# Kernel tuning notes

Hardware: AMD Instinct MI355X
Metric: run time of the kernel (lower is better)

## Reference

```python
import jax, jax.numpy as jnp
import numpy as np
from jax import lax

N_CLS = 4
ALPHA = 1.0
EPS = 1e-4


def _level_loss(logit, prob_gt, coord_gt, weight_cls):
    # logit: [B, N_cls*A, D, H, W]; prob_gt: [B, A, D, H, W]; coord_gt: [B, K, 4] int
    B, C, D, H, W = logit.shape
    A = C // N_CLS
    logit6 = logit.reshape(B, N_CLS, A, D, H, W)
    prob = jnp.clip(jax.nn.sigmoid(logit6), EPS, 1.0 - EPS)  # [B,N_cls,A,D,H,W]
    prob_max = jnp.max(prob, axis=1)                          # [B,A,D,H,W]

    # --- negative (background) focal term with NMS peak masking ---
    negmask = (prob_gt == -1.0).astype(logit.dtype)
    pooled = lax.reduce_window(prob_max, -jnp.inf, lax.max,
                               (1, 1, 3, 3, 3), (1, 1, 1, 1, 1),
                               [(0, 0), (0, 0), (1, 1), (1, 1), (1, 1)])
    max_filter = lax.stop_gradient((pooled == prob_max).astype(logit.dtype))
    thresh_filter = (prob_max > EPS).astype(logit.dtype)
    negmask = negmask * max_filter * thresh_filter
    w_neg = lax.stop_gradient(prob_max) ** ALPHA * negmask
    loss_neg = -jnp.sum(jnp.log(1.0 - prob_max) * w_neg)
    count_neg = jnp.sum(w_neg)

    # --- positive + other-class terms at sparse GT coordinates (vmapped over batch) ---
    def per_item(p_pred, l_pred, c_gt, p_gt):
        # p_pred/l_pred: [N_cls,A,D,H,W]; c_gt: [K,4]; p_gt: [A,D,H,W]
        valid = c_gt[:, 0] > -1
        vmask = valid.astype(p_pred.dtype)
        c = jnp.where(valid[:, None], c_gt, 0)  # safe indices for padded rows
        a, d, h, w = c[:, 0], c[:, 1], c[:, 2], c[:, 3]
        cls_gt = jnp.clip(p_gt[a, d, h, w].astype(jnp.int32) - 1, 0, N_CLS - 1)  # [K]
        p_t = p_pred[cls_gt, a, d, h, w]  # [K]
        l_t = l_pred[cls_gt, a, d, h, w]
        w_pos = (1.0 - lax.stop_gradient(p_t)) ** ALPHA * weight_cls[cls_gt] * vmask
        loss_pos = -jnp.sum(jax.nn.log_sigmoid(l_t) * w_pos)
        count_pos = jnp.sum(w_pos)
        # other-class suppression
        p_o = p_pred[:, a, d, h, w]  # [N_cls, K]
        l_o = l_pred[:, a, d, h, w]
        w_o = lax.stop_gradient(
            jax.nn.relu(p_o - (p_t - 0.05))
            * (p_o > 0.5).astype(p_o.dtype)
            * (p_t > 0.5).astype(p_o.dtype))
        # torch: weight[cls_gt] = 0  -> zero entire rows for classes present among valid GTs
        present = jnp.zeros((N_CLS,), p_pred.dtype).at[cls_gt].max(vmask)
        w_o = w_o * (1.0 - present)[:, None] * vmask[None, :]
        loss_other = jnp.sum(-jax.nn.log_sigmoid(-l_o) * w_o)
        count_other = jnp.sum(w_o)
        return loss_pos, count_pos, loss_other, count_other

    lp, cp, lo, co = jax.vmap(per_item)(prob, logit6, coord_gt, prob_gt)
    return (jnp.sum(lp), loss_neg, jnp.sum(lo), jnp.sum(cp), count_neg, jnp.sum(co))


def _forward(logits0, logits1, gtprob0, gtprob1, coords0, coords1, weight_cls):
    r0 = _level_loss(logits0, gtprob0, coords0, weight_cls)
    r1 = _level_loss(logits1, gtprob1, coords1, weight_cls)
    # [loss_pos, loss_neg, loss_other, count_pos, count_neg, count_other]
    return jnp.stack([a + b for a, b in zip(r0, r1)])


def setup_inputs() -> dict:
    rng = np.random.default_rng(0)
    B, A = 2, 2
    level_shapes = [(64, 128, 128), (32, 64, 64)]
    K, K_VALID = 32, 24
    out = {}
    for i, (D, H, W) in enumerate(level_shapes):
        logits = rng.standard_normal((B, N_CLS * A, D, H, W)).astype(np.float32)
        gt = -np.ones((B, A, D, H, W), np.float32)
        coords = -np.ones((B, K, 4), np.int32)
        for b in range(B):
            a = rng.integers(0, A, K_VALID)
            d = rng.integers(0, D, K_VALID)
            h = rng.integers(0, H, K_VALID)
            w = rng.integers(0, W, K_VALID)
            cls = rng.integers(1, N_CLS + 1, K_VALID)
            gt[b, a, d, h, w] = cls.astype(np.float32)
            coords[b, :K_VALID, 0] = a
            coords[b, :K_VALID, 1] = d
            coords[b, :K_VALID, 2] = h
            coords[b, :K_VALID, 3] = w
        out[f"logits{i}"] = jnp.asarray(logits)
        out[f"gtprob{i}"] = jnp.asarray(gt)
        out[f"coords{i}"] = jnp.asarray(coords)
    out["weight_cls"] = jnp.ones((N_CLS,), jnp.float32)
    return out


def reference(logits0, logits1, gtprob0, gtprob1, coords0, coords1, weight_cls):
    return _forward(logits0, logits1, gtprob0, gtprob1, coords0, coords1, weight_cls)
```

## Files before the change

### kernel.cpp

```cpp
#include <hip/hip_runtime.h>
#include <math.h>

#define EPSF 1e-4f
#define NB_L1 128
#define NB_L0 1024
#define NBLK (NB_L1 + NB_L0)

static __device__ __forceinline__ float sigmoid_fast(float x) {
    float e = __expf(-x);
    float p = __builtin_amdgcn_rcpf(1.0f + e);
    return fminf(fmaxf(p, EPSF), 1.0f - EPSF);
}
static __device__ __forceinline__ float sigmoid_precise(float x) {
    float p = 1.0f / (1.0f + expf(-x));
    return fminf(fmaxf(p, EPSF), 1.0f - EPSF);
}
static __device__ __forceinline__ float softplus(float x) {
    return fmaxf(x, 0.0f) + log1pf(expf(-fabsf(x)));
}
static __device__ __forceinline__ float4 fmax4(float4 a, float4 b) {
    float4 r;
    r.x = fmaxf(a.x, b.x); r.y = fmaxf(a.y, b.y);
    r.z = fmaxf(a.z, b.z); r.w = fmaxf(a.w, b.w);
    return r;
}
static __device__ __forceinline__ float4 sig4(float4 x) {
    float4 r;
    r.x = sigmoid_fast(x.x); r.y = sigmoid_fast(x.y);
    r.z = sigmoid_fast(x.z); r.w = sigmoid_fast(x.w);
    return r;
}

template <int WG, int Wc>
static __device__ __forceinline__ float4 wmax_row(const float* pm, int row, int w0) {
    const float4 v = *(const float4*)(pm + (size_t)row * Wc + 4 * w0);
    float lft = __shfl_up(v.w, 1);
    float rgt = __shfl_down(v.x, 1);
    lft = (w0 == 0) ? -INFINITY : lft;
    rgt = (w0 == WG - 1) ? -INFINITY : rgt;
    float4 r;
    r.x = fmaxf(fmaxf(lft, v.x), v.y);
    r.y = fmaxf(fmaxf(v.x, v.y), v.z);
    r.z = fmaxf(fmaxf(v.y, v.z), v.w);
    r.w = fmaxf(fmaxf(v.z, v.w), rgt);
    return r;
}
template <int WG, int Wc>
static __device__ __forceinline__ float4 hfold(const float* pm, int row0, int w0) {
    return fmax4(fmax4(wmax_row<WG, Wc>(pm, row0, w0), wmax_row<WG, Wc>(pm, row0 + 1, w0)),
                 wmax_row<WG, Wc>(pm, row0 + 2, w0));
}

template <int Wc, int TD, int TH, int D, int H>
static __device__ void neg_tile(const float* __restrict__ logits,
                                const float* __restrict__ gtprob,
                                int tileIdx, float* pm,
                                double& lsum, double& csum) {
    constexpr int WG = Wc / 4;
    constexpr int NROWH = TH + 2;
    constexpr int NROW = (TD + 2) * NROWH;
    constexpr int RPP = 512 / WG;
    constexpr int NPASS = (NROW + RPP - 1) / RPP;
    constexpr int NCELL = TD * TH;
    constexpr int CPT = (NCELL + RPP - 1) / RPP;
    constexpr int NH = H / TH, ND = D / TD;
    const int ht = tileIdx % NH;
    const int dt = (tileIdx / NH) % ND;
    const int ab = tileIdx / (NH * ND);
    const int a = ab & 1, b = ab >> 1;
    const int h0 = ht * TH, d0 = dt * TD;
    const size_t HW = (size_t)H * Wc;
    const size_t vol = (size_t)D * HW;
    const float* lg = logits + ((size_t)b * 8 + a) * vol;
    const size_t cs = 2 * vol;
    const float* gtb = gtprob + ((size_t)b * 2 + a) * vol;
    const int tid = threadIdx.x;
    const int w0 = tid % WG, rg = tid / WG;

    auto rowinfo = [&](int r, bool& inb) -> const float* {
        int rc = r < NROW - 1 ? r : NROW - 1;
        int rd = rc / NROWH, rh = rc - rd * NROWH;
        int d = d0 + rd - 1, h = h0 + rh - 1;
        inb = ((unsigned)d < (unsigned)D) & ((unsigned)h < (unsigned)H) & (r < NROW);
        int dc = d < 0 ? 0 : (d >= D ? D - 1 : d);
        int hc = h < 0 ? 0 : (h >= H ? H - 1 : h);
        return lg + (size_t)dc * HW + (size_t)hc * Wc + 4 * w0;
    };

    float4 n0, n1, n2, n3;
    bool ninb;
    {
        const float* p = rowinfo(rg, ninb);
        n0 = *(const float4*)p;            n1 = *(const float4*)(p + cs);
        n2 = *(const float4*)(p + 2 * cs); n3 = *(const float4*)(p + 3 * cs);
    }
#pragma unroll
    for (int ps = 0; ps < NPASS; ps++) {
        float4 c0 = n0, c1 = n1, c2 = n2, c3 = n3;
        bool inb = ninb;
        int r = rg + ps * RPP;
        if (ps + 1 < NPASS) {
            bool ib;
            const float* q = rowinfo(rg + (ps + 1) * RPP, ib);
            ninb = ib;
            n0 = *(const float4*)q;            n1 = *(const float4*)(q + cs);
            n2 = *(const float4*)(q + 2 * cs); n3 = *(const float4*)(q + 3 * cs);
        }
        float4 v = sig4(fmax4(fmax4(c0, c1), fmax4(c2, c3)));
        if (!inb) v = make_float4(-INFINITY, -INFINITY, -INFINITY, -INFINITY);
        if (r < NROW) *(float4*)(pm + (size_t)r * Wc + 4 * w0) = v;
    }

    float4 gq[CPT];
    int cdd[CPT], chh[CPT];
    bool cok[CPT];
#pragma unroll
    for (int k = 0; k < CPT; k++) {
        int cidx = rg + k * RPP;
        bool ok = cidx < NCELL;
        int ci = ok ? cidx : 0;
        int dd = ci / TH, hh = ci - dd * TH;
        cdd[k] = dd; chh[k] = hh; cok[k] = ok;
        gq[k] = *(const float4*)(gtb + (size_t)(d0 + dd) * HW + (size_t)(h0 + hh) * Wc + 4 * w0);
    }
    __syncthreads();

#pragma unroll
    for (int k = 0; k < CPT; k++) {
        if (!cok[k]) continue;
        int dd = cdd[k], hh = chh[k];
        float4 hm0 = hfold<WG, Wc>(pm, (dd + 0) * NROWH + hh, w0);
        float4 hm1 = hfold<WG, Wc>(pm, (dd + 1) * NROWH + hh, w0);
        float4 hm2 = hfold<WG, Wc>(pm, (dd + 2) * NROWH + hh, w0);
        float4 mx = fmax4(fmax4(hm0, hm1), hm2);
        float4 pc = *(const float4*)(pm + (size_t)((dd + 1) * NROWH + hh + 1) * Wc + 4 * w0);
        float4 g = gq[k];
        if (g.x == -1.0f && mx.x == pc.x && pc.x > EPSF) {
            lsum += (double)(-__logf(1.0f - pc.x) * pc.x); csum += (double)pc.x;
        }
        if (g.y == -1.0f && mx.y == pc.y && pc.y > EPSF) {
            lsum += (double)(-__logf(1.0f - pc.y) * pc.y); csum += (double)pc.y;
        }
        if (g.z == -1.0f && mx.z == pc.z && pc.z > EPSF) {
            lsum += (double)(-__logf(1.0f - pc.z) * pc.z); csum += (double)pc.z;
        }
        if (g.w == -1.0f && mx.w == pc.w && pc.w > EPSF) {
            lsum += (double)(-__logf(1.0f - pc.w) * pc.w); csum += (double)pc.w;
        }
    }
}

__global__ __launch_bounds__(512) void fused_kernel(
    const float* __restrict__ lg0, const float* __restrict__ gt0, const int* __restrict__ c0,
    const float* __restrict__ lg1, const float* __restrict__ gt1, const int* __restrict__ c1,
    const float* __restrict__ wcls, double* __restrict__ gacc) {
    __shared__ float pm[60 * 128];
    __shared__ double spart[48];
    __shared__ unsigned present[4];
    int tid = threadIdx.x;
    int bid = blockIdx.x;
    double v0 = 0, v1 = 0, v2 = 0, v3 = 0, v4 = 0, v5 = 0;

    if (bid >= NB_L1) {
        neg_tile<128, 4, 8, 64, 128>(lg0, gt0, bid - NB_L1, pm, v1, v4);
    } else {
        if (bid == 0) {
            if (tid < 4) present[tid] = 0u;
            __syncthreads();
            int lvl = (tid >> 6) & 1, tt = tid & 63;
            int b = tt >> 5, k = tt & 31;
            const float* lg = lvl ? lg1 : lg0;
            const float* gt = lvl ? gt1 : gt0;
            const int* cd = lvl ? c1 : c0;
            int D = lvl ? 32 : 64, H = lvl ? 64 : 128, Wd = lvl ? 64 : 128;
            int a = 0, d = 0, h = 0, w = 0, cls = 0;
            bool valid = false;
            size_t vol = (size_t)D * H * Wd, off = 0;
            if (tid < 128) {
                const int* c = cd + ((size_t)b * 32 + k) * 4;
                a = c[0]; d = c[1]; h = c[2]; w = c[3];
                valid = a > -1;
                if (!valid) { a = 0; d = 0; h = 0; w = 0; }
                off = ((size_t)d * H + h) * (size_t)Wd + w;
                float gval = gt[((size_t)b * 2 + a) * vol + off];
                cls = (int)gval - 1;
                cls = cls < 0 ? 0 : (cls > 3 ? 3 : cls);
                if (valid) atomicOr(&present[lvl * 2 + b], 1u << cls);
            }
            __syncthreads();
            if (tid < 128) {
                unsigned pmask = present[lvl * 2 + b];
                float vm = valid ? 1.0f : 0.0f;
                const float* lgb = lg + (size_t)b * 8 * vol;
                size_t aoff = (size_t)a * vol + off;
                float l_t = lgb[(size_t)cls * 2 * vol + aoff];
                float p_t = sigmoid_precise(l_t);
                float w_pos = (1.0f - p_t) * wcls[cls] * vm;
                float loss_pos = softplus(-l_t) * w_pos;
                float ptg = (p_t > 0.5f) ? 1.0f : 0.0f;
                float lo = 0.0f, co = 0.0f;
#pragma unroll
                for (int cc = 0; cc < 4; cc++) {
                    float l_o = lgb[(size_t)cc * 2 * vol + aoff];
                    float p_o = sigmoid_precise(l_o);
                    float wo = fmaxf(p_o - (p_t - 0.05f), 0.0f) * ((p_o > 0.5f) ? 1.0f : 0.0f) * ptg;
                    float pres = ((pmask >> cc) & 1u) ? 1.0f : 0.0f;
                    wo *= (1.0f - pres) * vm;
                    lo += softplus(l_o) * wo;
                    co += wo;
                }
                v0 = loss_pos; v3 = w_pos; v2 = lo; v5 = co;
            }
            __syncthreads();
        }
        neg_tile<64, 8, 8, 32, 64>(lg1, gt1, bid, pm, v1, v4);
    }

    for (int o = 32; o > 0; o >>= 1) {
        v1 += __shfl_down(v1, o);
        v4 += __shfl_down(v4, o);
    }
    if (bid == 0) {
        for (int o = 32; o > 0; o >>= 1) {
            v0 += __shfl_down(v0, o); v2 += __shfl_down(v2, o);
            v3 += __shfl_down(v3, o); v5 += __shfl_down(v5, o);
        }
    }
    int wave = tid >> 6, lane = tid & 63;
    if (lane == 0) {
        double* sp = spart + wave * 6;
        sp[0] = v0; sp[1] = v1; sp[2] = v2; sp[3] = v3; sp[4] = v4; sp[5] = v5;
    }
    __syncthreads();
    if (tid == 0) {
        double s1 = 0, s4 = 0;
#pragma unroll
        for (int wv = 0; wv < 8; wv++) { s1 += spart[wv * 6 + 1]; s4 += spart[wv * 6 + 4]; }
        atomicAdd(&gacc[1], s1);
        atomicAdd(&gacc[4], s4);
        if (bid == 0) {
            double s0 = 0, s2 = 0, s3 = 0, s5 = 0;
#pragma unroll
            for (int wv = 0; wv < 8; wv++) {
                s0 += spart[wv * 6 + 0]; s2 += spart[wv * 6 + 2];
                s3 += spart[wv * 6 + 3]; s5 += spart[wv * 6 + 5];
            }
            atomicAdd(&gacc[0], s0); atomicAdd(&gacc[2], s2);
            atomicAdd(&gacc[3], s3); atomicAdd(&gacc[5], s5);
        }
    }
}

__global__ void finalize_kernel(const double* __restrict__ gacc, float* __restrict__ out) {
    int i = threadIdx.x;
    if (i < 6) out[i] = (float)gacc[i];
}

extern "C" void kernel_launch(void* const* d_in, const int* in_sizes, int n_in,
                              void* d_out, int out_size, void* d_ws, size_t ws_size,
                              hipStream_t stream) {
    const float *logits0 = nullptr, *gtprob0 = nullptr, *logits1 = nullptr,
                *gtprob1 = nullptr, *wcls = nullptr;
    const int *coords0 = nullptr, *coords1 = nullptr;
    for (int i = 0; i < n_in; i++) {
        switch (in_sizes[i]) {
            case 16777216: logits0 = (const float*)d_in[i]; break;
            case 4194304:  gtprob0 = (const float*)d_in[i]; break;
            case 2097152:  logits1 = (const float*)d_in[i]; break;
            case 524288:   gtprob1 = (const float*)d_in[i]; break;
            case 4:        wcls    = (const float*)d_in[i]; break;
            case 256:
                if (!coords0) coords0 = (const int*)d_in[i];
                else          coords1 = (const int*)d_in[i];
                break;
        }
    }
    double* gacc = (double*)d_ws;
    hipMemsetAsync(d_ws, 0, 6 * sizeof(double), stream);
    fused_kernel<<<NBLK, 512, 0, stream>>>(logits0, gtprob0, coords0,
                                           logits1, gtprob1, coords1,
                                           wcls, gacc);
    finalize_kernel<<<1, 64, 0, stream>>>(gacc, (float*)d_out);
}
```

Measured before the change: 146.8 us.

## Persistent blocks process three tiles with double-buffered LDS and deferred sigmoid

Cuts the grid to 512 blocks. Each block handles two level-0 tiles and one level-1 tile, and double-buffers shared memory so global loads for the next tile are issued while the current tile's NMS compute runs. Sigmoid is now applied only to surviving peak candidates instead of every loaded element, which relies on sigmoid being monotonic for the max comparison. This adds register pressure (large payload arrays), launch_bounds(512,4) and doubled LDS. The clamp-at-EPS equality semantics could change slightly because max is compared on raw logits.

```diff
diff --git a/kernel.cpp b/kernel.cpp
--- a/kernel.cpp
+++ b/kernel.cpp
@@ -2,9 +2,7 @@
 #include <math.h>
 
 #define EPSF 1e-4f
-#define NB_L1 128
-#define NB_L0 1024
-#define NBLK (NB_L1 + NB_L0)
+#define NBLK 512
 
 static __device__ __forceinline__ float sigmoid_fast(float x) {
     float e = __expf(-x);
@@ -22,12 +20,6 @@
     float4 r;
     r.x = fmaxf(a.x, b.x); r.y = fmaxf(a.y, b.y);
     r.z = fmaxf(a.z, b.z); r.w = fmaxf(a.w, b.w);
-    return r;
-}
-static __device__ __forceinline__ float4 sig4(float4 x) {
-    float4 r;
-    r.x = sigmoid_fast(x.x); r.y = sigmoid_fast(x.y);
-    r.z = sigmoid_fast(x.z); r.w = sigmoid_fast(x.w);
     return r;
 }
 
@@ -52,169 +44,217 @@
 }
 
 template <int Wc, int TD, int TH, int D, int H>
-static __device__ void neg_tile(const float* __restrict__ logits,
-                                const float* __restrict__ gtprob,
-                                int tileIdx, float* pm,
-                                double& lsum, double& csum) {
-    constexpr int WG = Wc / 4;
-    constexpr int NROWH = TH + 2;
-    constexpr int NROW = (TD + 2) * NROWH;
-    constexpr int RPP = 512 / WG;
-    constexpr int NPASS = (NROW + RPP - 1) / RPP;
-    constexpr int NCELL = TD * TH;
-    constexpr int CPT = (NCELL + RPP - 1) / RPP;
+static __device__ __forceinline__ void tile_decode(
+    int tileIdx, int& d0, int& h0, const float*& lg, const float*& gtb,
+    const float* logits, const float* gtprob) {
     constexpr int NH = H / TH, ND = D / TD;
-    const int ht = tileIdx % NH;
-    const int dt = (tileIdx / NH) % ND;
-    const int ab = tileIdx / (NH * ND);
-    const int a = ab & 1, b = ab >> 1;
-    const int h0 = ht * TH, d0 = dt * TD;
-    const size_t HW = (size_t)H * Wc;
-    const size_t vol = (size_t)D * HW;
-    const float* lg = logits + ((size_t)b * 8 + a) * vol;
-    const size_t cs = 2 * vol;
-    const float* gtb = gtprob + ((size_t)b * 2 + a) * vol;
-    const int tid = threadIdx.x;
-    const int w0 = tid % WG, rg = tid / WG;
-
-    auto rowinfo = [&](int r, bool& inb) -> const float* {
-        int rc = r < NROW - 1 ? r : NROW - 1;
+    int ht = tileIdx % NH;
+    int dt = (tileIdx / NH) % ND;
+    int ab = tileIdx / (NH * ND);
+    int a = ab & 1, b = ab >> 1;
+    h0 = ht * TH; d0 = dt * TD;
+    size_t HW = (size_t)H * Wc, vol = (size_t)D * HW;
+    lg = logits + ((size_t)b * 8 + a) * vol;
+    gtb = gtprob + ((size_t)b * 2 + a) * vol;
+}
+
+template <int Wc, int TD, int TH, int D, int H, int NPASS>
+static __device__ __forceinline__ void fill_issue(
+    const float* lg, int d0, int h0, int tid, float4* pay, bool* pinb) {
+    constexpr int WG = Wc / 4, NROWH = TH + 2, NROW = (TD + 2) * NROWH, RPP = 512 / WG;
+    const size_t HW = (size_t)H * Wc, cs = 2 * (size_t)D * HW;
+    const int w0 = tid % WG, rg = tid / WG;
+#pragma unroll
+    for (int ps = 0; ps < NPASS; ps++) {
+        int r = rg + ps * RPP;
+        int rc = r < NROW ? r : NROW - 1;
         int rd = rc / NROWH, rh = rc - rd * NROWH;
         int d = d0 + rd - 1, h = h0 + rh - 1;
-        inb = ((unsigned)d < (unsigned)D) & ((unsigned)h < (unsigned)H) & (r < NROW);
+        pinb[ps] = ((unsigned)d < (unsigned)D) & ((unsigned)h < (unsigned)H) & (r < NROW);
         int dc = d < 0 ? 0 : (d >= D ? D - 1 : d);
         int hc = h < 0 ? 0 : (h >= H ? H - 1 : h);
-        return lg + (size_t)dc * HW + (size_t)hc * Wc + 4 * w0;
-    };
-
-    float4 n0, n1, n2, n3;
-    bool ninb;
-    {
-        const float* p = rowinfo(rg, ninb);
-        n0 = *(const float4*)p;            n1 = *(const float4*)(p + cs);
-        n2 = *(const float4*)(p + 2 * cs); n3 = *(const float4*)(p + 3 * cs);
-    }
+        const float* p = lg + (size_t)dc * HW + (size_t)hc * Wc + 4 * w0;
+        pay[ps * 4 + 0] = *(const float4*)(p);
+        pay[ps * 4 + 1] = *(const float4*)(p + cs);
+        pay[ps * 4 + 2] = *(const float4*)(p + 2 * cs);
+        pay[ps * 4 + 3] = *(const float4*)(p + 3 * cs);
+    }
+}
+
+template <int Wc, int TD, int TH, int NPASS>
+static __device__ __forceinline__ void fill_write(
+    float* buf, int tid, const float4* pay, const bool* pinb) {
+    constexpr int WG = Wc / 4, NROWH = TH + 2, NROW = (TD + 2) * NROWH, RPP = 512 / WG;
+    const int w0 = tid % WG, rg = tid / WG;
 #pragma unroll
     for (int ps = 0; ps < NPASS; ps++) {
-        float4 c0 = n0, c1 = n1, c2 = n2, c3 = n3;
-        bool inb = ninb;
         int r = rg + ps * RPP;
-        if (ps + 1 < NPASS) {
-            bool ib;
-            const float* q = rowinfo(rg + (ps + 1) * RPP, ib);
-            ninb = ib;
-            n0 = *(const float4*)q;            n1 = *(const float4*)(q + cs);
-            n2 = *(const float4*)(q + 2 * cs); n3 = *(const float4*)(q + 3 * cs);
-        }
-        float4 v = sig4(fmax4(fmax4(c0, c1), fmax4(c2, c3)));
-        if (!inb) v = make_float4(-INFINITY, -INFINITY, -INFINITY, -INFINITY);
-        if (r < NROW) *(float4*)(pm + (size_t)r * Wc + 4 * w0) = v;
-    }
-
-    float4 gq[CPT];
-    int cdd[CPT], chh[CPT];
-    bool cok[CPT];
+        float4 v = fmax4(fmax4(pay[ps * 4 + 0], pay[ps * 4 + 1]),
+                         fmax4(pay[ps * 4 + 2], pay[ps * 4 + 3]));
+        if (!pinb[ps]) v = make_float4(-INFINITY, -INFINITY, -INFINITY, -INFINITY);
+        if (r < NROW) *(float4*)(buf + (size_t)r * Wc + 4 * w0) = v;
+    }
+}
+
+template <int Wc, int TD, int TH, int D, int H, int CPT>
+static __device__ __forceinline__ void gt_issue(
+    const float* gtb, int d0, int h0, int tid, float4* gq) {
+    constexpr int WG = Wc / 4, RPP = 512 / WG, NCELL = TD * TH;
+    const size_t HW = (size_t)H * Wc;
+    const int w0 = tid % WG, rg = tid / WG;
 #pragma unroll
     for (int k = 0; k < CPT; k++) {
         int cidx = rg + k * RPP;
-        bool ok = cidx < NCELL;
-        int ci = ok ? cidx : 0;
+        int ci = cidx < NCELL ? cidx : 0;
         int dd = ci / TH, hh = ci - dd * TH;
-        cdd[k] = dd; chh[k] = hh; cok[k] = ok;
         gq[k] = *(const float4*)(gtb + (size_t)(d0 + dd) * HW + (size_t)(h0 + hh) * Wc + 4 * w0);
     }
-    __syncthreads();
-
-#pragma unroll
-    for (int k = 0; k < CPT; k++) {
-        if (!cok[k]) continue;
-        int dd = cdd[k], hh = chh[k];
-        float4 hm0 = hfold<WG, Wc>(pm, (dd + 0) * NROWH + hh, w0);
-        float4 hm1 = hfold<WG, Wc>(pm, (dd + 1) * NROWH + hh, w0);
-        float4 hm2 = hfold<WG, Wc>(pm, (dd + 2) * NROWH + hh, w0);
-        float4 mx = fmax4(fmax4(hm0, hm1), hm2);
-        float4 pc = *(const float4*)(pm + (size_t)((dd + 1) * NROWH + hh + 1) * Wc + 4 * w0);
-        float4 g = gq[k];
-        if (g.x == -1.0f && mx.x == pc.x && pc.x > EPSF) {
-            lsum += (double)(-__logf(1.0f - pc.x) * pc.x); csum += (double)pc.x;
-        }
-        if (g.y == -1.0f && mx.y == pc.y && pc.y > EPSF) {
-            lsum += (double)(-__logf(1.0f - pc.y) * pc.y); csum += (double)pc.y;
-        }
-        if (g.z == -1.0f && mx.z == pc.z && pc.z > EPSF) {
-            lsum += (double)(-__logf(1.0f - pc.z) * pc.z); csum += (double)pc.z;
-        }
-        if (g.w == -1.0f && mx.w == pc.w && pc.w > EPSF) {
-            lsum += (double)(-__logf(1.0f - pc.w) * pc.w); csum += (double)pc.w;
-        }
-    }
-}
-
-__global__ __launch_bounds__(512) void fused_kernel(
+}
+
+static __device__ __forceinline__ void neg_accum(
+    float g, float mx, float pc, double& lsum, double& csum) {
+    if (g == -1.0f && mx == pc) {
+        float p = sigmoid_fast(pc);
+        if (p > EPSF) {
+            lsum += (double)(-__logf(1.0f - p) * p);
+            csum += (double)p;
+        }
+    }
+}
+
+template <int Wc, int TH>
+static __device__ __forceinline__ void compute_pair(
+    const float* buf, int tid, const float4* gq, double& ls, double& cs) {
+    constexpr int WG = Wc / 4, NROWH = TH + 2;
+    const int w0 = tid % WG, rg = tid / WG;
+    const int dd = rg >> 3, hh = rg & 7;
+    float4 f0 = hfold<WG, Wc>(buf, (dd + 0) * NROWH + hh, w0);
+    float4 f1 = hfold<WG, Wc>(buf, (dd + 1) * NROWH + hh, w0);
+    float4 f2 = hfold<WG, Wc>(buf, (dd + 2) * NROWH + hh, w0);
+    float4 f3 = hfold<WG, Wc>(buf, (dd + 3) * NROWH + hh, w0);
+    float4 f4 = hfold<WG, Wc>(buf, (dd + 4) * NROWH + hh, w0);
+    float4 mx0 = fmax4(fmax4(f0, f1), f2);
+    float4 mx1 = fmax4(fmax4(f2, f3), f4);
+    float4 pc0 = *(const float4*)(buf + (size_t)((dd + 1) * NROWH + hh + 1) * Wc + 4 * w0);
+    float4 pc1 = *(const float4*)(buf + (size_t)((dd + 3) * NROWH + hh + 1) * Wc + 4 * w0);
+    neg_accum(gq[0].x, mx0.x, pc0.x, ls, cs);
+    neg_accum(gq[0].y, mx0.y, pc0.y, ls, cs);
+    neg_accum(gq[0].z, mx0.z, pc0.z, ls, cs);
+    neg_accum(gq[0].w, mx0.w, pc0.w, ls, cs);
+    neg_accum(gq[1].x, mx1.x, pc1.x, ls, cs);
+    neg_accum(gq[1].y, mx1.y, pc1.y, ls, cs);
+    neg_accum(gq[1].z, mx1.z, pc1.z, ls, cs);
+    neg_accum(gq[1].w, mx1.w, pc1.w, ls, cs);
+}
+
+template <int Wc, int TD, int TH>
+static __device__ __forceinline__ void compute_single(
+    const float* buf, int tid, const float4* gq, double& ls, double& cs) {
+    constexpr int WG = Wc / 4, NROWH = TH + 2, NCELL = TD * TH;
+    const int w0 = tid % WG, rg = tid / WG;
+    if (rg < NCELL) {
+        int dd = rg / TH, hh = rg - dd * TH;
+        float4 f0 = hfold<WG, Wc>(buf, (dd + 0) * NROWH + hh, w0);
+        float4 f1 = hfold<WG, Wc>(buf, (dd + 1) * NROWH + hh, w0);
+        float4 f2 = hfold<WG, Wc>(buf, (dd + 2) * NROWH + hh, w0);
+        float4 mx = fmax4(fmax4(f0, f1), f2);
+        float4 pc = *(const float4*)(buf + (size_t)((dd + 1) * NROWH + hh + 1) * Wc + 4 * w0);
+        neg_accum(gq[0].x, mx.x, pc.x, ls, cs);
+        neg_accum(gq[0].y, mx.y, pc.y, ls, cs);
+        neg_accum(gq[0].z, mx.z, pc.z, ls, cs);
+        neg_accum(gq[0].w, mx.w, pc.w, ls, cs);
+    }
+}
+
+__global__ __launch_bounds__(512, 4) void fused_kernel(
     const float* __restrict__ lg0, const float* __restrict__ gt0, const int* __restrict__ c0,
     const float* __restrict__ lg1, const float* __restrict__ gt1, const int* __restrict__ c1,
     const float* __restrict__ wcls, double* __restrict__ gacc) {
-    __shared__ float pm[60 * 128];
+    __shared__ float buf0[60 * 128];
+    __shared__ float buf1[60 * 128];
     __shared__ double spart[48];
     __shared__ unsigned present[4];
-    int tid = threadIdx.x;
-    int bid = blockIdx.x;
+    const int tid = threadIdx.x;
+    const int bid = blockIdx.x;
     double v0 = 0, v1 = 0, v2 = 0, v3 = 0, v4 = 0, v5 = 0;
 
-    if (bid >= NB_L1) {
-        neg_tile<128, 4, 8, 64, 128>(lg0, gt0, bid - NB_L1, pm, v1, v4);
-    } else {
-        if (bid == 0) {
-            if (tid < 4) present[tid] = 0u;
-            __syncthreads();
-            int lvl = (tid >> 6) & 1, tt = tid & 63;
-            int b = tt >> 5, k = tt & 31;
-            const float* lg = lvl ? lg1 : lg0;
-            const float* gt = lvl ? gt1 : gt0;
-            const int* cd = lvl ? c1 : c0;
-            int D = lvl ? 32 : 64, H = lvl ? 64 : 128, Wd = lvl ? 64 : 128;
-            int a = 0, d = 0, h = 0, w = 0, cls = 0;
-            bool valid = false;
-            size_t vol = (size_t)D * H * Wd, off = 0;
-            if (tid < 128) {
-                const int* c = cd + ((size_t)b * 32 + k) * 4;
-                a = c[0]; d = c[1]; h = c[2]; w = c[3];
-                valid = a > -1;
-                if (!valid) { a = 0; d = 0; h = 0; w = 0; }
-                off = ((size_t)d * H + h) * (size_t)Wd + w;
-                float gval = gt[((size_t)b * 2 + a) * vol + off];
-                cls = (int)gval - 1;
-                cls = cls < 0 ? 0 : (cls > 3 ? 3 : cls);
-                if (valid) atomicOr(&present[lvl * 2 + b], 1u << cls);
+    if (bid == 0) {
+        if (tid < 4) present[tid] = 0u;
+        __syncthreads();
+        int lvl = (tid >> 6) & 1, tt = tid & 63;
+        int b = tt >> 5, k = tt & 31;
+        const float* lg = lvl ? lg1 : lg0;
+        const float* gt = lvl ? gt1 : gt0;
+        const int* cd = lvl ? c1 : c0;
+        int D = lvl ? 32 : 64, H = lvl ? 64 : 128, Wd = lvl ? 64 : 128;
+        int a = 0, d = 0, h = 0, w = 0, cls = 0;
+        bool valid = false;
+        size_t vol = (size_t)D * H * Wd, off = 0;
+        if (tid < 128) {
+            const int* c = cd + ((size_t)b * 32 + k) * 4;
+            a = c[0]; d = c[1]; h = c[2]; w = c[3];
+            valid = a > -1;
+            if (!valid) { a = 0; d = 0; h = 0; w = 0; }
+            off = ((size_t)d * H + h) * (size_t)Wd + w;
+            float gval = gt[((size_t)b * 2 + a) * vol + off];
+            cls = (int)gval - 1;
+            cls = cls < 0 ? 0 : (cls > 3 ? 3 : cls);
+            if (valid) atomicOr(&present[lvl * 2 + b], 1u << cls);
+        }
+        __syncthreads();
+        if (tid < 128) {
+            unsigned pmask = present[lvl * 2 + b];
+            float vm = valid ? 1.0f : 0.0f;
+            const float* lgb = lg + (size_t)b * 8 * vol;
+            size_t aoff = (size_t)a * vol + off;
+            float l_t = lgb[(size_t)cls * 2 * vol + aoff];
+            float p_t = sigmoid_precise(l_t);
+            float w_pos = (1.0f - p_t) * wcls[cls] * vm;
+            float loss_pos = softplus(-l_t) * w_pos;
+            float ptg = (p_t > 0.5f) ? 1.0f : 0.0f;
+            float lo = 0.0f, co = 0.0f;
+#pragma unroll
+            for (int cc = 0; cc < 4; cc++) {
+                float l_o = lgb[(size_t)cc * 2 * vol + aoff];
+                float p_o = sigmoid_precise(l_o);
+                float wo = fmaxf(p_o - (p_t - 0.05f), 0.0f) * ((p_o > 0.5f) ? 1.0f : 0.0f) * ptg;
+                float pres = ((pmask >> cc) & 1u) ? 1.0f : 0.0f;
+                wo *= (1.0f - pres) * vm;
+                lo += softplus(l_o) * wo;
+                co += wo;
             }
-            __syncthreads();
-            if (tid < 128) {
-                unsigned pmask = present[lvl * 2 + b];
-                float vm = valid ? 1.0f : 0.0f;
-                const float* lgb = lg + (size_t)b * 8 * vol;
-                size_t aoff = (size_t)a * vol + off;
-                float l_t = lgb[(size_t)cls * 2 * vol + aoff];
-                float p_t = sigmoid_precise(l_t);
-                float w_pos = (1.0f - p_t) * wcls[cls] * vm;
-                float loss_pos = softplus(-l_t) * w_pos;
-                float ptg = (p_t > 0.5f) ? 1.0f : 0.0f;
-                float lo = 0.0f, co = 0.0f;
-#pragma unroll
-                for (int cc = 0; cc < 4; cc++) {
-                    float l_o = lgb[(size_t)cc * 2 * vol + aoff];
-                    float p_o = sigmoid_precise(l_o);
-                    float wo = fmaxf(p_o - (p_t - 0.05f), 0.0f) * ((p_o > 0.5f) ? 1.0f : 0.0f) * ptg;
-                    float pres = ((pmask >> cc) & 1u) ? 1.0f : 0.0f;
-                    wo *= (1.0f - pres) * vm;
-                    lo += softplus(l_o) * wo;
-                    co += wo;
-                }
-                v0 = loss_pos; v3 = w_pos; v2 = lo; v5 = co;
-            }
-            __syncthreads();
-        }
-        neg_tile<64, 8, 8, 32, 64>(lg1, gt1, bid, pm, v1, v4);
-    }
+            v0 = loss_pos; v3 = w_pos; v2 = lo; v5 = co;
+        }
+        __syncthreads();
+    }
+
+    int d0a, h0a; const float *lgA, *gtA;
+    tile_decode<128, 4, 8, 64, 128>(2 * bid, d0a, h0a, lgA, gtA, lg0, gt0);
+    float4 payA[16]; bool inbA[4]; float4 gqA[2];
+    fill_issue<128, 4, 8, 64, 128, 4>(lgA, d0a, h0a, tid, payA, inbA);
+    gt_issue<128, 4, 8, 64, 128, 2>(gtA, d0a, h0a, tid, gqA);
+    fill_write<128, 4, 8, 4>(buf0, tid, payA, inbA);
+    __syncthreads();
+
+    int d0b, h0b; const float *lgB, *gtB;
+    tile_decode<128, 4, 8, 64, 128>(2 * bid + 1, d0b, h0b, lgB, gtB, lg0, gt0);
+    float4 payB[16]; bool inbB[4]; float4 gqB[2];
+    fill_issue<128, 4, 8, 64, 128, 4>(lgB, d0b, h0b, tid, payB, inbB);
+    gt_issue<128, 4, 8, 64, 128, 2>(gtB, d0b, h0b, tid, gqB);
+    compute_pair<128, 8>(buf0, tid, gqA, v1, v4);
+    fill_write<128, 4, 8, 4>(buf1, tid, payB, inbB);
+    __syncthreads();
+
+    int d0c, h0c; const float *lgC, *gtC;
+    tile_decode<64, 2, 8, 32, 64>(bid, d0c, h0c, lgC, gtC, lg1, gt1);
+    float4 payC[8]; bool inbC[2]; float4 gqC[1];
+    fill_issue<64, 2, 8, 32, 64, 2>(lgC, d0c, h0c, tid, payC, inbC);
+    gt_issue<64, 2, 8, 32, 64, 1>(gtC, d0c, h0c, tid, gqC);
+    compute_pair<128, 8>(buf1, tid, gqB, v1, v4);
+    fill_write<64, 2, 8, 2>(buf0, tid, payC, inbC);
+    __syncthreads();
+
+    compute_single<64, 2, 8>(buf0, tid, gqC, v1, v4);
 
     for (int o = 32; o > 0; o >>= 1) {
         v1 += __shfl_down(v1, o);
```

Measured after the change: 176.3 us. 20.1% more time.
